# Kernel tuning notes

Hardware: AMD Instinct MI355X
Metric: run time of the kernel (lower is better)

Reference implementation:

```python
import jax, jax.numpy as jnp
import numpy as np

B, S, E, H = 2, 2048, 1024, 16
HD = E // H
DFF = 4 * E
LN_EPS = 1e-5


def _layernorm(x, g, b):
    mu = jnp.mean(x, axis=-1, keepdims=True)
    var = jnp.mean(jnp.square(x - mu), axis=-1, keepdims=True)
    return (x - mu) * jax.lax.rsqrt(var + LN_EPS) * g + b


def setup_inputs() -> dict:
    key = jax.random.key(0)
    ks = jax.random.split(key, 6)
    inp = {
        "x": jax.random.normal(ks[0], (B, S, E), jnp.float32),
        "ln1_g": jnp.ones((E,), jnp.float32),
        "ln1_b": jnp.zeros((E,), jnp.float32),
        "ln2_g": jnp.ones((E,), jnp.float32),
        "ln2_b": jnp.zeros((E,), jnp.float32),
        # OptimizedPoincareBallLinear init: randn * 0.1, zero bias
        "w_qkv": jax.random.normal(ks[1], (3 * E, E), jnp.float32) * 0.1,
        "b_qkv": jnp.zeros((3 * E,), jnp.float32),
        "w_ao": jax.random.normal(ks[2], (E, E), jnp.float32) * 0.1,
        "b_ao": jnp.zeros((E,), jnp.float32),
        "w_fc": jax.random.normal(ks[3], (DFF, E), jnp.float32) * 0.1,
        "b_fc": jnp.zeros((DFF,), jnp.float32),
        "w_po": jax.random.normal(ks[4], (E, DFF), jnp.float32) * 0.1,
        "b_po": jnp.zeros((E,), jnp.float32),
    }
    return inp


def reference(x, ln1_g, ln1_b, ln2_g, ln2_b, w_qkv, b_qkv, w_ao, b_ao,
              w_fc, b_fc, w_po, b_po):
    # --- attention branch ---
    h = _layernorm(x, ln1_g, ln1_b)
    qkv = h @ w_qkv.T + b_qkv                       # [B,S,3E]
    qkv = qkv.reshape(B, S, H, 3 * HD).transpose(0, 2, 1, 3)  # [B,H,S,3hd]
    q, k, v = jnp.split(qkv, 3, axis=-1)            # each [B,H,S,hd]
    scores = jnp.einsum('bhqd,bhkd->bhqk', q, k) / jnp.sqrt(
        jnp.asarray(HD, jnp.float32))
    causal = jnp.tril(jnp.ones((S, S), bool))        # attn_bias[:, :, :S, :S]
    scores = jnp.where(causal, scores, jnp.finfo(scores.dtype).min)
    attn_w = jax.nn.softmax(scores, axis=-1)         # dropout p=0.1 inactive (eval)
    attn = jnp.einsum('bhqk,bhkd->bhqd', attn_w, v)  # [B,H,S,hd]
    attn = attn.transpose(0, 2, 1, 3).reshape(B, S, E)
    attn = attn @ w_ao.T + b_ao
    x = x + attn
    # --- MLP branch ---
    h2 = _layernorm(x, ln2_g, ln2_b)
    h2 = h2 @ w_fc.T + b_fc
    h2 = jax.nn.gelu(h2, approximate=True)           # GPT-2 gelu_new
    h2 = h2 @ w_po.T + b_po
    x = x + h2
    return x
```

## Files before the change

### kernel.cpp

```cpp
#include <hip/hip_runtime.h>
#include <cstddef>
#include <cstdint>

#define Bc 2
#define Sc 2048
#define Ec 1024
#define Hc 16
#define HDc 64
#define DFFc 4096
#define ROWS (Bc * Sc)

typedef _Float16 half8v __attribute__((ext_vector_type(8)));
typedef _Float16 half4v __attribute__((ext_vector_type(4)));
typedef float f32x4 __attribute__((ext_vector_type(4)));
typedef _Float16 h16;

__device__ inline void gld_lds16(const void* g, void* l) {
    __builtin_amdgcn_global_load_lds(
        (const __attribute__((address_space(1))) void*)g,
        (__attribute__((address_space(3))) void*)l, 16, 0, 0);
}

__device__ inline float exp2_fast(float x) {
    float r;
    asm("v_exp_f32 %0, %1" : "=v"(r) : "v"(x));
    return r;
}

__device__ inline float gelu_new(float x) {
    float x2 = x * x;
    float u = x * fmaf(0.07135481627362f, x2, 1.5957691216057308f);
    return x / (1.0f + __expf(-u));
}

__global__ __launch_bounds__(256) void cvt4_kernel(
    const float* __restrict__ a,
    const float* __restrict__ b,
    const float* __restrict__ c,
    const float* __restrict__ d,
    h16* __restrict__ out)
{
    int bid = blockIdx.x;
    const float* src;
    size_t obase;
    int base;
    if (bid < 3072)      { src = a; obase = 0;       base = bid; }
    else if (bid < 4096) { src = b; obase = 3145728; base = bid - 3072; }
    else if (bid < 8192) { src = c; obase = 4194304; base = bid - 4096; }
    else                 { src = d; obase = 8388608; base = bid - 8192; }
    int i = base * 1024 + threadIdx.x * 4;
    float4 v = *(const float4*)(src + i);
    half4v o;
    o.x = (h16)v.x; o.y = (h16)v.y; o.z = (h16)v.z; o.w = (h16)v.w;
    *(half4v*)(out + obase + i) = o;
}

__device__ inline float block_sum256(float v, float* sb) {
    #pragma unroll
    for (int o = 32; o > 0; o >>= 1) v += __shfl_down(v, o, 64);
    int lane = threadIdx.x & 63, w = threadIdx.x >> 6;
    if (lane == 0) sb[w] = v;
    __syncthreads();
    float r = sb[0] + sb[1] + sb[2] + sb[3];
    __syncthreads();
    return r;
}

__global__ __launch_bounds__(256) void ln_kernel(const float* __restrict__ x,
                                                 const float* __restrict__ g,
                                                 const float* __restrict__ b,
                                                 h16* __restrict__ out) {
    __shared__ float sb[4];
    int row = blockIdx.x;
    int t = threadIdx.x;
    const float* xr = x + (size_t)row * Ec;
    float4 v = ((const float4*)xr)[t];
    float s = v.x + v.y + v.z + v.w;
    float mu = block_sum256(s, sb) * (1.0f / Ec);
    float dx = v.x - mu, dy = v.y - mu, dz = v.z - mu, dw = v.w - mu;
    float ss = dx * dx + dy * dy + dz * dz + dw * dw;
    float var = block_sum256(ss, sb) * (1.0f / Ec);
    float inv = rsqrtf(var + 1e-5f);
    float4 gv = ((const float4*)g)[t];
    float4 bv = ((const float4*)b)[t];
    half4v o;
    o.x = (h16)(dx * inv * gv.x + bv.x);
    o.y = (h16)(dy * inv * gv.y + bv.y);
    o.z = (h16)(dz * inv * gv.z + bv.z);
    o.w = (h16)(dw * inv * gv.w + bv.w);
    ((half4v*)(out + (size_t)row * Ec))[t] = o;
}

template <int EPI, typename OutT>
__global__ __launch_bounds__(512, 2) void gemm_8w(
    const h16* __restrict__ A, const h16* __restrict__ W,
    const float* __restrict__ bias, const float* __restrict__ R,
    OutT* __restrict__ C, int M, int N, int K, int lda)
{
    __shared__ h16 S[4][16384];

    const int tid = threadIdx.x;
    const int lane = tid & 63, wv = tid >> 6;
    const int wm = wv >> 2, wn = wv & 3;
    const int c15 = lane & 15, q = lane >> 4;

    const int cpx = gridDim.x >> 3;
    const int wg = ((int)blockIdx.x & 7) * cpx + ((int)blockIdx.x >> 3);
    int r0, c0, sp = 0;
    if (EPI == 3) {
        sp = wg >> 6;
        int rem = wg & 63;
        r0 = (rem >> 2) << 8;
        c0 = (rem & 3) << 8;
    } else {
        const int nbn = N >> 8;
        r0 = (wg / nbn) << 8;
        c0 = (wg % nbn) << 8;
    }

    const int gc8 = (tid & 3) ^ ((tid >> 3) & 3);
    const h16* gA = A + (size_t)(r0 + (tid >> 2)) * lda + sp * 1024 + gc8 * 8;
    const h16* gB = W + (size_t)(c0 + (tid >> 2)) * lda + sp * 1024 + gc8 * 8;
    const size_t hK = (size_t)128 * lda;

    int aoff[8], boff[4];
    #pragma unroll
    for (int m = 0; m < 8; ++m) {
        int row = wm * 128 + m * 16 + c15;
        aoff[m] = row * 32 + ((q ^ ((row >> 1) & 3)) << 3);
    }
    #pragma unroll
    for (int n = 0; n < 4; ++n) {
        int row = wn * 64 + n * 16 + c15;
        boff[n] = 8192 + row * 32 + ((q ^ ((row >> 1) & 3)) << 3);
    }

    f32x4 acc[8][4];
    #pragma unroll
    for (int m = 0; m < 8; ++m)
        #pragma unroll
        for (int n = 0; n < 4; ++n)
            acc[m][n] = (f32x4){0.f, 0.f, 0.f, 0.f};

    const int NT = K >> 5;

    auto stage4 = [&](int tt) {
        h16* b = &S[tt & 3][0];
        const h16* a = gA + tt * 32;
        const h16* w = gB + tt * 32;
        gld_lds16(a,      b + tid * 8);
        gld_lds16(a + hK, b + 4096 + tid * 8);
        gld_lds16(w,      b + 8192 + tid * 8);
        gld_lds16(w + hK, b + 12288 + tid * 8);
    };

    half8v afloA[4], bfA[4], afloB[4], bfB[4];

    auto step = [&](int s, half8v (&aflo)[4], half8v (&bf)[4],
                    half8v (&aflo2)[4], half8v (&bf2)[4]) {
        if (s + 3 < NT) stage4(s + 3);
        if (s + 3 < NT)      asm volatile("s_waitcnt vmcnt(8)" ::: "memory");
        else if (s + 2 < NT) asm volatile("s_waitcnt vmcnt(4)" ::: "memory");
        else if (s + 1 < NT) asm volatile("s_waitcnt vmcnt(0)" ::: "memory");
        if (s + 1 < NT) {
            asm volatile("s_waitcnt lgkmcnt(0)" ::: "memory");
            __builtin_amdgcn_s_barrier();
        }
        const h16* b = &S[s & 3][0];
        half8v ah[4];
        #pragma unroll
        for (int m = 0; m < 4; ++m) ah[m] = *(const half8v*)(b + aoff[4 + m]);

        __builtin_amdgcn_s_setprio(1);
        #pragma unroll
        for (int m = 0; m < 4; ++m)
            #pragma unroll
            for (int n = 0; n < 4; ++n)
                acc[m][n] = __builtin_amdgcn_mfma_f32_16x16x32_f16(aflo[m], bf[n], acc[m][n], 0, 0, 0);
        __builtin_amdgcn_s_setprio(0);

        if (s + 1 < NT) {
            const h16* b2 = &S[(s + 1) & 3][0];
            #pragma unroll
            for (int m = 0; m < 4; ++m) aflo2[m] = *(const half8v*)(b2 + aoff[m]);
            #pragma unroll
            for (int n = 0; n < 4; ++n) bf2[n]  = *(const half8v*)(b2 + boff[n]);
        }

        __builtin_amdgcn_s_setprio(1);
        #pragma unroll
        for (int m = 0; m < 4; ++m)
            #pragma unroll
            for (int n = 0; n < 4; ++n)
                acc[4 + m][n] = __builtin_amdgcn_mfma_f32_16x16x32_f16(ah[m], bf[n], acc[4 + m][n], 0, 0, 0);
        __builtin_amdgcn_s_setprio(0);
    };

    stage4(0); stage4(1); stage4(2);
    asm volatile("s_waitcnt vmcnt(8)" ::: "memory");
    __builtin_amdgcn_s_barrier();
    {
        const h16* b0 = &S[0][0];
        #pragma unroll
        for (int m = 0; m < 4; ++m) afloA[m] = *(const half8v*)(b0 + aoff[m]);
        #pragma unroll
        for (int n = 0; n < 4; ++n) bfA[n] = *(const half8v*)(b0 + boff[n]);
    }

    for (int t = 0; t < NT; t += 2) {
        step(t,     afloA, bfA, afloB, bfB);
        step(t + 1, afloB, bfB, afloA, bfA);
    }

    h16* Pp = nullptr;
    if (EPI == 3 && sp < 3) {
        size_t po = (sp == 0) ? 0 : (sp == 1) ? 8388608u : 25165824u;
        Pp = (h16*)((char*)(void*)R + po);
    }
    float bvs[4];
    #pragma unroll
    for (int n = 0; n < 4; ++n) bvs[n] = bias[c0 + wn * 64 + n * 16 + c15];
    #pragma unroll
    for (int m = 0; m < 8; ++m) {
        #pragma unroll
        for (int n = 0; n < 4; ++n) {
            int col = c0 + wn * 64 + n * 16 + c15;
            #pragma unroll
            for (int r = 0; r < 4; ++r) {
                int row = r0 + wm * 128 + m * 16 + q * 4 + r;
                size_t off = (size_t)row * N + col;
                if (EPI == 3) {
                    float v = acc[m][n][r];
                    if (sp < 3) Pp[off] = (h16)v;
                    else ((float*)C)[off] = v;
                } else {
                    float v = acc[m][n][r] + bvs[n];
                    if (EPI == 1) v += R[off];
                    if (EPI == 2) v = gelu_new(v);
                    if (sizeof(OutT) == 2) ((h16*)C)[off] = (h16)v;
                    else ((float*)C)[off] = v;
                }
            }
        }
    }
}

__global__ __launch_bounds__(256) void red3_kernel(
    const h16* __restrict__ P0, const h16* __restrict__ P1,
    const h16* __restrict__ P2, const float* __restrict__ xr,
    const float* __restrict__ bias, float* __restrict__ out)
{
    size_t i = ((size_t)blockIdx.x * 256 + threadIdx.x) * 8;
    int col = (int)(i & 1023);
    half8v p0 = *(const half8v*)(P0 + i);
    half8v p1 = *(const half8v*)(P1 + i);
    half8v p2 = *(const half8v*)(P2 + i);
    float4 x0 = *(const float4*)(xr + i);
    float4 x1v = *(const float4*)(xr + i + 4);
    float4 b0 = *(const float4*)(bias + col);
    float4 b1 = *(const float4*)(bias + col + 4);
    float4 o0 = *(const float4*)(out + i);
    float4 o1 = *(const float4*)(out + i + 4);
    float ps[8];
    #pragma unroll
    for (int u = 0; u < 8; ++u)
        ps[u] = (float)p0[u] + (float)p1[u] + (float)p2[u];
    o0.x += x0.x + b0.x + ps[0];
    o0.y += x0.y + b0.y + ps[1];
    o0.z += x0.z + b0.z + ps[2];
    o0.w += x0.w + b0.w + ps[3];
    o1.x += x1v.x + b1.x + ps[4];
    o1.y += x1v.y + b1.y + ps[5];
    o1.z += x1v.z + b1.z + ps[6];
    o1.w += x1v.w + b1.w + ps[7];
    *(float4*)(out + i) = o0;
    *(float4*)(out + i + 4) = o1;
}

template <int EPI, typename OutT>
__global__ __launch_bounds__(256, 2) void gemm_k64(
    const h16* __restrict__ A, const h16* __restrict__ W,
    const float* __restrict__ bias, const float* __restrict__ R,
    OutT* __restrict__ C, int M, int N, int K)
{
    __shared__ h16 S[4][6144];

    const int t = threadIdx.x;
    const int lane = t & 63, wv = t >> 6;
    const int wm = wv >> 1, wn = wv & 1;
    const int c15 = lane & 15, q = lane >> 4;
    const int id = blockIdx.x;
    const int cx = id & 7;
    const int kq = id >> 3;
    const int bx = kq & 7;
    const int by = ((kq >> 3) << 3) | cx;
    const int row0 = by * 64, col0 = bx * 128;

    const int gc8 = (t & 3) ^ ((t >> 3) & 3);
    const h16* gA  = A + (size_t)(row0 + (t >> 2)) * K + gc8 * 8;
    const h16* gB0 = W + (size_t)(col0 + (t >> 2)) * K + gc8 * 8;
    const h16* gB1 = gB0 + (size_t)64 * K;

    int aoff[2], boff[4];
    #pragma unroll
    for (int i = 0; i < 2; ++i) {
        int row = wm * 32 + i * 16 + c15;
        aoff[i] = row * 32 + ((q ^ ((row >> 1) & 3)) << 3);
    }
    #pragma unroll
    for (int j = 0; j < 4; ++j) {
        int row = wn * 64 + j * 16 + c15;
        boff[j] = 2048 + row * 32 + ((q ^ ((row >> 1) & 3)) << 3);
    }

    f32x4 acc[2][4];
    #pragma unroll
    for (int i = 0; i < 2; ++i)
        #pragma unroll
        for (int j = 0; j < 4; ++j)
            acc[i][j] = (f32x4){0.f, 0.f, 0.f, 0.f};

    const int NT = K >> 5;

    auto stage = [&](int tt) {
        h16* b = &S[tt & 3][0];
        gld_lds16(gA  + tt * 32, b + t * 8);
        gld_lds16(gB0 + tt * 32, b + 2048 + t * 8);
        gld_lds16(gB1 + tt * 32, b + 4096 + t * 8);
    };

    stage(0); stage(1); stage(2);
    asm volatile("s_waitcnt vmcnt(6)" ::: "memory");
    __builtin_amdgcn_s_barrier();

    for (int tt = 0; tt < NT; ++tt) {
        if (tt + 3 < NT) stage(tt + 3);

        const h16* b = &S[tt & 3][0];
        half8v af[2], bf[4];
        #pragma unroll
        for (int i = 0; i < 2; ++i) af[i] = *(const half8v*)(b + aoff[i]);
        #pragma unroll
        for (int j = 0; j < 4; ++j) bf[j] = *(const half8v*)(b + boff[j]);

        __builtin_amdgcn_s_setprio(1);
        #pragma unroll
        for (int i = 0; i < 2; ++i)
            #pragma unroll
            for (int j = 0; j < 4; ++j)
                acc[i][j] = __builtin_amdgcn_mfma_f32_16x16x32_f16(af[i], bf[j], acc[i][j], 0, 0, 0);
        __builtin_amdgcn_s_setprio(0);

        if (tt < NT - 1) {
            if (tt + 3 < NT)       asm volatile("s_waitcnt vmcnt(6)" ::: "memory");
            else if (tt + 3 == NT) asm volatile("s_waitcnt vmcnt(3)" ::: "memory");
            else                   asm volatile("s_waitcnt vmcnt(0)" ::: "memory");
            __builtin_amdgcn_s_barrier();
        }
    }

    #pragma unroll
    for (int i = 0; i < 2; ++i) {
        #pragma unroll
        for (int j = 0; j < 4; ++j) {
            int col = col0 + wn * 64 + j * 16 + c15;
            float bv = bias[col];
            #pragma unroll
            for (int r = 0; r < 4; ++r) {
                int row = row0 + wm * 32 + i * 16 + q * 4 + r;
                size_t off = (size_t)row * N + col;
                float v = acc[i][j][r] + bv;
                if (EPI == 1) v += R[off];
                if (EPI == 2) v = gelu_new(v);
                if (sizeof(OutT) == 2) ((h16*)C)[off] = (h16)v;
                else ((float*)C)[off] = v;
            }
        }
    }
}

__global__ __launch_bounds__(256, 4) void attn_mfma(const h16* __restrict__ qkv,
                                                    h16* __restrict__ attn) {
    __shared__ h16 Ks[2][2][64 * 32];
    __shared__ h16 Vt[2][64 * 32];
    __shared__ h16 Ps[4][16 * 72];

    const int t = threadIdx.x;
    const int lane = t & 63, wv = t >> 6;
    const int c15 = lane & 15, q = lane >> 4;
    const int bh = blockIdx.x, b = bh >> 4, h = bh & 15;
    const int ja = 31 - blockIdx.y;
    const int qbase = ja * 64 + wv * 16;
    const int SE = 3 * Ec;
    const size_t hbase = (size_t)b * Sc * SE + (size_t)h * (3 * HDc);

    const int krow = t >> 2;
    const int kcol = (((t & 3) ^ ((t >> 3) & 3)) << 3);
    const int vkey = t & 31, vd0 = (t >> 5) << 3;
    half8v vreg[2];

    const int ksw = (q ^ ((c15 >> 1) & 3)) << 3;
    int vaddr[8];
    #pragma unroll
    for (int u = 0; u < 8; ++u) {
        int d = vd0 + u;
        vaddr[u] = d * 32 + (((vkey >> 3) ^ ((d >> 1) & 3)) << 3) + (vkey & 7);
    }

    half8v qf[2];
    #pragma unroll
    for (int kk = 0; kk < 2; ++kk) {
        qf[kk] = *(const half8v*)(qkv + hbase + (size_t)(qbase + c15) * SE + kk * 32 + q * 8);
        qf[kk] *= (h16)0.18033688f;
    }

    f32x4 O[4];
    #pragma unroll
    for (int n = 0; n < 4; ++n) O[n] = (f32x4){0.f, 0.f, 0.f, 0.f};
    float mi = -3e38f, li = 0.f;

    auto stageK = [&](int kt, int bf) {
        #pragma unroll
        for (int p = 0; p < 2; ++p)
            gld_lds16(qkv + hbase + (size_t)(kt * 64 + krow) * SE + HDc + p * 32 + kcol,
                      &Ks[bf][p][krow * 32 + ((t & 3) << 3)]);
    };
    auto loadV = [&](int kt) {
        #pragma unroll
        for (int p = 0; p < 2; ++p)
            vreg[p] = *(const half8v*)(qkv + hbase +
                        (size_t)(kt * 64 + p * 32 + vkey) * SE + 2 * HDc + vd0);
    };
    auto scatV = [&]() {
        #pragma unroll
        for (int p = 0; p < 2; ++p)
            #pragma unroll
            for (int u = 0; u < 8; ++u)
                Vt[p][vaddr[u]] = vreg[p][u];
    };

    stageK(0, 0);
    loadV(0);
    scatV();
    __syncthreads();

    for (int kt = 0; kt <= ja; ++kt) {
        const int bf = kt & 1;
        if (kt < ja) { stageK(kt + 1, bf ^ 1); loadV(kt + 1); }

        f32x4 st[4];
        #pragma unroll
        for (int j = 0; j < 4; ++j) {
            half8v kf0 = *(const half8v*)&Ks[bf][0][(j * 16 + c15) * 32 + ksw];
            half8v kf1 = *(const half8v*)&Ks[bf][1][(j * 16 + c15) * 32 + ksw];
            f32x4 z = (f32x4){0.f, 0.f, 0.f, 0.f};
            z = __builtin_amdgcn_mfma_f32_16x16x32_f16(kf0, qf[0], z, 0, 0, 0);
            st[j] = __builtin_amdgcn_mfma_f32_16x16x32_f16(kf1, qf[1], z, 0, 0, 0);
        }

        if (kt == ja) {
            const int rowloc = wv * 16 + c15;
            #pragma unroll
            for (int j = 0; j < 4; ++j)
                #pragma unroll
                for (int r = 0; r < 4; ++r)
                    if (j * 16 + q * 4 + r > rowloc) st[j][r] = -3e38f;
        }

        float mx = mi;
        #pragma unroll
        for (int j = 0; j < 4; ++j)
            #pragma unroll
            for (int r = 0; r < 4; ++r) mx = fmaxf(mx, st[j][r]);
        mx = fmaxf(mx, __shfl_xor(mx, 16, 64));
        mx = fmaxf(mx, __shfl_xor(mx, 32, 64));
        float al = exp2_fast(mi - mx);
        mi = mx;
        float ps = 0.f;
        #pragma unroll
        for (int j = 0; j < 4; ++j) {
            half4v pk;
            #pragma unroll
            for (int r = 0; r < 4; ++r) {
                float p = exp2_fast(st[j][r] - mx);
                ps += p;
                pk[r] = (h16)p;
            }
            *(half4v*)&Ps[wv][c15 * 72 + j * 16 + q * 4] = pk;
        }
        ps += __shfl_xor(ps, 16, 64);
        ps += __shfl_xor(ps, 32, 64);
        li = li * al + ps;

        half8v pb0 = *(const half8v*)&Ps[wv][c15 * 72 + q * 8];
        half8v pb1 = *(const half8v*)&Ps[wv][c15 * 72 + 32 + q * 8];
        #pragma unroll
        for (int n = 0; n < 4; ++n) {
            #pragma unroll
            for (int r = 0; r < 4; ++r) O[n][r] *= al;
            half8v va0 = *(const half8v*)&Vt[0][(n * 16 + c15) * 32 + ksw];
            half8v va1 = *(const half8v*)&Vt[1][(n * 16 + c15) * 32 + ksw];
            O[n] = __builtin_amdgcn_mfma_f32_16x16x32_f16(va0, pb0, O[n], 0, 0, 0);
            O[n] = __builtin_amdgcn_mfma_f32_16x16x32_f16(va1, pb1, O[n], 0, 0, 0);
        }

        if (kt < ja) {
            __syncthreads();
            scatV();
            __syncthreads();
        }
    }

    float rl = 1.0f / li;
    #pragma unroll
    for (int n = 0; n < 4; ++n) {
        half4v o4;
        #pragma unroll
        for (int r = 0; r < 4; ++r) o4[r] = (h16)(O[n][r] * rl);
        *(half4v*)(attn + ((size_t)(b * Sc + qbase + c15)) * Ec + h * HDc + n * 16 + q * 4) = o4;
    }
}

extern "C" void kernel_launch(void* const* d_in, const int* in_sizes, int n_in,
                              void* d_out, int out_size, void* d_ws, size_t ws_size,
                              hipStream_t stream) {
    const float* x     = (const float*)d_in[0];
    const float* ln1_g = (const float*)d_in[1];
    const float* ln1_b = (const float*)d_in[2];
    const float* ln2_g = (const float*)d_in[3];
    const float* ln2_b = (const float*)d_in[4];
    const float* w_qkv = (const float*)d_in[5];
    const float* b_qkv = (const float*)d_in[6];
    const float* w_ao  = (const float*)d_in[7];
    const float* b_ao  = (const float*)d_in[8];
    const float* w_fc  = (const float*)d_in[9];
    const float* b_fc  = (const float*)d_in[10];
    const float* w_po  = (const float*)d_in[11];
    const float* b_po  = (const float*)d_in[12];
    float* out = (float*)d_out;

    char* w = (char*)d_ws;
    h16* wqkv = (h16*)(w);
    h16* wao  = (h16*)(w + 6291456);
    h16* wfc  = (h16*)(w + 8388608);
    h16* wpo  = (h16*)(w + 16777216);
    h16* hb   = (h16*)(w + 25165824);
    h16* qkv  = (h16*)(w + 33554432);
    h16* attn = (h16*)(w + 58720256);
    float* x1 = (float*)(w + 67108864);
    h16* ff   = qkv;

    dim3 blk(256);
    dim3 blk8(512);

    cvt4_kernel<<<dim3(12288), blk, 0, stream>>>(w_qkv, w_ao, w_fc, w_po, wqkv);

    ln_kernel<<<dim3(ROWS), blk, 0, stream>>>(x, ln1_g, ln1_b, hb);
    gemm_8w<0, h16><<<dim3((ROWS / 256) * (3 * Ec / 256)), blk8, 0, stream>>>(
        hb, wqkv, b_qkv, nullptr, qkv, ROWS, 3 * Ec, Ec, Ec);
    attn_mfma<<<dim3(Bc * Hc, 32), blk, 0, stream>>>(qkv, attn);
    gemm_k64<1, float><<<dim3(512), blk, 0, stream>>>(
        attn, wao, b_ao, x, x1, ROWS, Ec, Ec);
    ln_kernel<<<dim3(ROWS), blk, 0, stream>>>(x1, ln2_g, ln2_b, hb);
    gemm_8w<2, h16><<<dim3((ROWS / 256) * (DFFc / 256)), blk8, 0, stream>>>(
        hb, wfc, b_fc, nullptr, ff, ROWS, DFFc, Ec, Ec);
    gemm_8w<3, float><<<dim3(256), blk8, 0, stream>>>(
        ff, wpo, b_po, (const float*)w, out, ROWS, Ec, 1024, DFFc);
    red3_kernel<<<dim3(2048), blk, 0, stream>>>(
        (const h16*)w, (const h16*)(w + 8388608), (const h16*)(w + 25165824),
        x1, b_po, out);
}
```

Baseline: 333.2 us.

## Double-buffer V tile in attention and use lazy softmax rescaling

Adds a second LDS buffer for the transposed V tile so the next tile can be scattered while the current one is consumed. This cuts the per-iteration barriers from two to one. It also adds a lazy online-softmax update: the running max and the O/l rescale change only when some lane's tile max exceeds the stored max by more than a threshold, skipping the per-tile exp and multiply on O. In exchange LDS use grows, which may lower occupancy, and exp values can reach up to 2^7 in fp16 P, trading some precision headroom.

```diff
diff --git a/kernel.cpp b/kernel.cpp
--- a/kernel.cpp
+++ b/kernel.cpp
@@ -382,7 +382,7 @@
 __global__ __launch_bounds__(256, 4) void attn_mfma(const h16* __restrict__ qkv,
                                                     h16* __restrict__ attn) {
     __shared__ h16 Ks[2][2][64 * 32];
-    __shared__ h16 Vt[2][64 * 32];
+    __shared__ h16 Vt[2][2][64 * 32];
     __shared__ h16 Ps[4][16 * 72];
 
     const int t = threadIdx.x;
@@ -431,21 +431,22 @@
             vreg[p] = *(const half8v*)(qkv + hbase +
                         (size_t)(kt * 64 + p * 32 + vkey) * SE + 2 * HDc + vd0);
     };
-    auto scatV = [&]() {
+    auto scatV = [&](int bf) {
         #pragma unroll
         for (int p = 0; p < 2; ++p)
             #pragma unroll
             for (int u = 0; u < 8; ++u)
-                Vt[p][vaddr[u]] = vreg[p][u];
+                Vt[bf][p][vaddr[u]] = vreg[p][u];
     };
 
     stageK(0, 0);
     loadV(0);
-    scatV();
-    __syncthreads();
+    scatV(0);
 
     for (int kt = 0; kt <= ja; ++kt) {
         const int bf = kt & 1;
+        __syncthreads();
+
         if (kt < ja) { stageK(kt + 1, bf ^ 1); loadV(kt + 1); }
 
         f32x4 st[4];
@@ -467,22 +468,30 @@
                     if (j * 16 + q * 4 + r > rowloc) st[j][r] = -3e38f;
         }
 
-        float mx = mi;
+        float mxt = st[0][0];
         #pragma unroll
         for (int j = 0; j < 4; ++j)
             #pragma unroll
-            for (int r = 0; r < 4; ++r) mx = fmaxf(mx, st[j][r]);
-        mx = fmaxf(mx, __shfl_xor(mx, 16, 64));
-        mx = fmaxf(mx, __shfl_xor(mx, 32, 64));
-        float al = exp2_fast(mi - mx);
-        mi = mx;
+            for (int r = 0; r < 4; ++r) mxt = fmaxf(mxt, st[j][r]);
+        mxt = fmaxf(mxt, __shfl_xor(mxt, 16, 64));
+        mxt = fmaxf(mxt, __shfl_xor(mxt, 32, 64));
+        if (!__all(mxt <= mi + 7.0f)) {
+            float mxn = fmaxf(mi, mxt);
+            float al = exp2_fast(mi - mxn);
+            mi = mxn;
+            li *= al;
+            #pragma unroll
+            for (int n = 0; n < 4; ++n)
+                #pragma unroll
+                for (int r = 0; r < 4; ++r) O[n][r] *= al;
+        }
         float ps = 0.f;
         #pragma unroll
         for (int j = 0; j < 4; ++j) {
             half4v pk;
             #pragma unroll
             for (int r = 0; r < 4; ++r) {
-                float p = exp2_fast(st[j][r] - mx);
+                float p = exp2_fast(st[j][r] - mi);
                 ps += p;
                 pk[r] = (h16)p;
             }
@@ -490,25 +499,19 @@
         }
         ps += __shfl_xor(ps, 16, 64);
         ps += __shfl_xor(ps, 32, 64);
-        li = li * al + ps;
+        li += ps;
 
         half8v pb0 = *(const half8v*)&Ps[wv][c15 * 72 + q * 8];
         half8v pb1 = *(const half8v*)&Ps[wv][c15 * 72 + 32 + q * 8];
         #pragma unroll
         for (int n = 0; n < 4; ++n) {
-            #pragma unroll
-            for (int r = 0; r < 4; ++r) O[n][r] *= al;
-            half8v va0 = *(const half8v*)&Vt[0][(n * 16 + c15) * 32 + ksw];
-            half8v va1 = *(const half8v*)&Vt[1][(n * 16 + c15) * 32 + ksw];
+            half8v va0 = *(const half8v*)&Vt[bf][0][(n * 16 + c15) * 32 + ksw];
+            half8v va1 = *(const half8v*)&Vt[bf][1][(n * 16 + c15) * 32 + ksw];
             O[n] = __builtin_amdgcn_mfma_f32_16x16x32_f16(va0, pb0, O[n], 0, 0, 0);
             O[n] = __builtin_amdgcn_mfma_f32_16x16x32_f16(va1, pb1, O[n], 0, 0, 0);
         }
 
-        if (kt < ja) {
-            __syncthreads();
-            scatV();
-            __syncthreads();
-        }
+        if (kt < ja) scatV(bf ^ 1);
     }
 
     float rl = 1.0f / li;
```

After: 327.9 us. No clear change (-1.6%).
